# Performance work log

Measured on AMD Instinct MI355X. Metric: run time of the kernel, lower is better.

## Reference

```python
import jax, jax.numpy as jnp
import numpy as np

N, D_IN, D_OUT = 4096, 1024, 1024

def setup_inputs() -> dict:
    key = jax.random.key(0)
    ks = jax.random.split(key, 7)
    s = 1.0 / np.sqrt(D_IN)
    return {
        "x": jax.random.normal(ks[0], (N, D_IN), dtype=jnp.float32),
        "W1": jax.random.normal(ks[1], (D_OUT, D_IN), dtype=jnp.float32) * s,
        "b1": jax.random.normal(ks[2], (D_OUT,), dtype=jnp.float32) * 0.01,
        "W2": jax.random.normal(ks[3], (D_OUT, D_IN), dtype=jnp.float32) * s,
        "b2": jax.random.normal(ks[4], (D_OUT,), dtype=jnp.float32) * 0.01,
        "W3": jax.random.normal(ks[5], (D_OUT, D_IN), dtype=jnp.float32) * s,
        "b3": jax.random.normal(ks[6], (D_OUT,), dtype=jnp.float32) * 0.01,
        "output_dim": D_OUT,
    }

def reference(x, W1, b1, W2, b2, W3, b3, output_dim):
    # q, k, v: [N, D_OUT]  (torch Linear: x @ W.T + b)
    q = x @ W1.T + b1
    k = x @ W2.T + b2
    v = x @ W3.T + b3
    # NOTE: original computes K @ Q^T (not Q @ K^T) — keep faithful.
    scale = 1.0 / jnp.sqrt(jnp.asarray(output_dim, dtype=x.dtype))
    attn = jax.nn.softmax(jnp.einsum("nd,md->nm", k, q) * scale, axis=-1)  # [N, N]
    # value.unsqueeze(0) * attn.unsqueeze(-1) summed over axis 1 == attn @ v
    return attn @ v  # [N, D_OUT]
```

## Files before the change

kernel.cpp:

```cpp
#include <hip/hip_runtime.h>


typedef short bf16x8 __attribute__((ext_vector_type(8)));
typedef float f32x4  __attribute__((ext_vector_type(4)));

struct FalseT { static constexpr bool value = false; };
struct TrueT  { static constexpr bool value = true;  };

__device__ __forceinline__ short f2bf(float f) {
    unsigned u = __builtin_bit_cast(unsigned, f);
    u += 0x7FFFu + ((u >> 16) & 1u);
    return (short)(u >> 16);
}
__device__ __forceinline__ float bf2f(short s) {
    return __builtin_bit_cast(float, (unsigned)((unsigned short)s) << 16);
}

__device__ __forceinline__ void gld_lds16(const short* g, short* l) {
    __builtin_amdgcn_global_load_lds(
        (const __attribute__((address_space(1))) void*)g,
        (__attribute__((address_space(3))) void*)l, 16, 0, 0);
}

#define WAITV(n) asm volatile("s_waitcnt vmcnt(" #n ")" ::: "memory")
#define BAR()    __builtin_amdgcn_s_barrier()

template<int CMODE>
__global__ __launch_bounds__(512)
void gemm256(const short* __restrict__ A, int lda,
             const short* __restrict__ B, int ldb,
             const float* __restrict__ bias,
             short* __restrict__ Cout, int ldc, float scale,
             int K, size_t zstride)
{
    __shared__ __align__(16) short As[2][2][128 * 64];
    __shared__ __align__(16) short Bs[2][2][128 * 64];

    const int tid  = threadIdx.x;
    const int lane = tid & 63;
    const int wave = tid >> 6;
    const int wr   = wave >> 2;
    const int wc   = wave & 3;
    const int quad = lane >> 4;
    const int l16  = lane & 15;
    const size_t bm0 = (size_t)blockIdx.y * 256;
    const size_t bn0 = (size_t)blockIdx.x * 256;
    const int koff = blockIdx.z * K;

    f32x4 acc[8][4] = {};

    const int srow  = lane >> 3;
    const int sgran = (lane & 7) ^ srow;
    const short* Ag0 = A + (bm0 + wave * 16 + srow) * (size_t)lda + koff + sgran * 8;
    const short* Ag1 = Ag0 + (size_t)128 * lda;
    const short* Bg0 = B + (bn0 + wave * 16 + srow) * (size_t)ldb + koff + sgran * 8;
    const short* Bg1 = Bg0 + (size_t)128 * ldb;

    const int s0   = ((quad ^ (l16 & 7)) << 3);
    const int s1   = (((4 + quad) ^ (l16 & 7)) << 3);
    const int rdA0 = (wr * 64 + l16) * 64;
    const int rdB0 = (wc * 32 + l16) * 64;

    auto stage = [&](short* half, const short* g, int ld, int kt) {
#pragma unroll
        for (int i = 0; i < 2; ++i)
            gld_lds16(g + (size_t)(i * 8) * ld + kt,
                      half + (wave * 16 + i * 8) * 64);
    };

    bf16x8 af[4][2], bfr0[2][2], bfr1[2][2];

    auto ldA = [&](const short* Ah, int ks, int soff) {
#pragma unroll
        for (int m4 = 0; m4 < 4; ++m4)
            af[m4][ks] = *(const bf16x8*)(Ah + rdA0 + m4 * 1024 + soff);
    };
    auto ldB = [&](bf16x8 (&bx)[2][2], const short* Bh, int ks, int soff) {
#pragma unroll
        for (int n2 = 0; n2 < 2; ++n2)
            bx[n2][ks] = *(const bf16x8*)(Bh + rdB0 + n2 * 1024 + soff);
    };
    auto mmks = [&](int mq, int nq, bf16x8 (&bx)[2][2], int ks) {
#pragma unroll
        for (int m4 = 0; m4 < 4; ++m4)
#pragma unroll
            for (int n2 = 0; n2 < 2; ++n2)
                acc[mq * 4 + m4][nq * 2 + n2] =
                    __builtin_amdgcn_mfma_f32_16x16x32_bf16(
                        af[m4][ks], bx[n2][ks],
                        acc[mq * 4 + m4][nq * 2 + n2], 0, 0, 0);
    };

    stage(&As[0][0][0], Ag0, lda, 0);
    stage(&Bs[0][0][0], Bg0, ldb, 0);
    stage(&Bs[0][1][0], Bg1, ldb, 0);
    stage(&As[0][1][0], Ag1, lda, 0);
    stage(&As[1][0][0], Ag0, lda, 64);
    stage(&Bs[1][0][0], Bg0, ldb, 64);
    stage(&Bs[1][1][0], Bg1, ldb, 64);
    WAITV(6);
    BAR();
    __builtin_amdgcn_sched_barrier(0);

    int kt = 0;
    auto iterbody = [&](auto LASTC) {
        constexpr bool LAST = decltype(LASTC)::value;
        ldB(bfr0, &Bs[0][0][0], 0, s0);
        ldA(&As[0][0][0], 0, s0);
        ldB(bfr0, &Bs[0][0][0], 1, s1);
        ldA(&As[0][0][0], 1, s1);
        stage(&As[1][1][0], Ag1, lda, kt + 64);
        __builtin_amdgcn_s_setprio(1);
        mmks(0, 0, bfr0, 0); mmks(0, 0, bfr0, 1);
        __builtin_amdgcn_s_setprio(0);
        BAR();
        ldB(bfr1, &Bs[0][1][0], 0, s0);
        ldB(bfr1, &Bs[0][1][0], 1, s1);
        if constexpr (!LAST) stage(&As[0][0][0], Ag0, lda, kt + 128);
        __builtin_amdgcn_s_setprio(1);
        mmks(0, 1, bfr1, 0); mmks(0, 1, bfr1, 1);
        __builtin_amdgcn_s_setprio(0);
        BAR();
        ldA(&As[0][1][0], 0, s0);
        ldA(&As[0][1][0], 1, s1);
        if constexpr (!LAST) stage(&Bs[0][0][0], Bg0, ldb, kt + 128);
        __builtin_amdgcn_s_setprio(1);
        mmks(1, 1, bfr1, 0); mmks(1, 1, bfr1, 1);
        __builtin_amdgcn_s_setprio(0);
        BAR();
        if constexpr (!LAST) stage(&Bs[0][1][0], Bg1, ldb, kt + 128);
        __builtin_amdgcn_s_setprio(1);
        mmks(1, 0, bfr0, 0); mmks(1, 0, bfr0, 1);
        __builtin_amdgcn_s_setprio(0);
        if constexpr (LAST) { WAITV(0); } else { WAITV(6); }
        __builtin_amdgcn_sched_barrier(0);
        BAR();
        ldB(bfr0, &Bs[1][0][0], 0, s0);
        ldA(&As[1][0][0], 0, s0);
        ldB(bfr0, &Bs[1][0][0], 1, s1);
        ldA(&As[1][0][0], 1, s1);
        if constexpr (!LAST) stage(&As[0][1][0], Ag1, lda, kt + 128);
        __builtin_amdgcn_s_setprio(1);
        mmks(0, 0, bfr0, 0); mmks(0, 0, bfr0, 1);
        __builtin_amdgcn_s_setprio(0);
        BAR();
        ldB(bfr1, &Bs[1][1][0], 0, s0);
        ldB(bfr1, &Bs[1][1][0], 1, s1);
        if constexpr (!LAST) stage(&As[1][0][0], Ag0, lda, kt + 192);
        __builtin_amdgcn_s_setprio(1);
        mmks(0, 1, bfr1, 0); mmks(0, 1, bfr1, 1);
        __builtin_amdgcn_s_setprio(0);
        BAR();
        ldA(&As[1][1][0], 0, s0);
        ldA(&As[1][1][0], 1, s1);
        if constexpr (!LAST) stage(&Bs[1][0][0], Bg0, ldb, kt + 192);
        __builtin_amdgcn_s_setprio(1);
        mmks(1, 1, bfr1, 0); mmks(1, 1, bfr1, 1);
        __builtin_amdgcn_s_setprio(0);
        BAR();
        if constexpr (!LAST) stage(&Bs[1][1][0], Bg1, ldb, kt + 192);
        __builtin_amdgcn_s_setprio(1);
        mmks(1, 0, bfr0, 0); mmks(1, 0, bfr0, 1);
        __builtin_amdgcn_s_setprio(0);
        if constexpr (!LAST) {
            WAITV(6);
            __builtin_amdgcn_sched_barrier(0);
        }
        BAR();
    };

    const int nfull = (K >> 7) - 1;
    for (int i = 0; i < nfull; ++i) {
        iterbody(FalseT{});
        kt += 128;
    }
    iterbody(TrueT{});

    short* Cs = Cout + ((CMODE == 3) ? (size_t)blockIdx.z * zstride : 0);
#pragma unroll
    for (int mt = 0; mt < 8; ++mt) {
        const int mq = mt >> 2, m4 = mt & 3;
#pragma unroll
        for (int nt = 0; nt < 4; ++nt) {
            const int nq = nt >> 1, n2 = nt & 1;
            const size_t col = bn0 + nq * 128 + wc * 32 + n2 * 16 + l16;
            const float bc = (CMODE == 0) ? bias[col] : 0.0f;
#pragma unroll
            for (int r = 0; r < 4; ++r) {
                const size_t row = bm0 + mq * 128 + wr * 64 + m4 * 16 + quad * 4 + r;
                float v = acc[mt][nt][r] * scale + bc;
                if (CMODE == 2) v = __expf(v);
                Cs[row * (size_t)ldc + col] = f2bf(v);
            }
        }
    }
}

__global__ __launch_bounds__(256)
void transpose_v(const short* __restrict__ qkv, short* __restrict__ vt)
{
    __shared__ short sh[64][72];
    const int n0 = blockIdx.x * 64, d0 = blockIdx.y * 64;
    const int t = threadIdx.x;
    const int r = t >> 2, c = (t & 3) << 4;

    const short* src = qkv + (size_t)(n0 + r) * 3072 + 2048 + d0 + c;
    *(int4*)(&sh[r][c])     = *(const int4*)(src);
    *(int4*)(&sh[r][c + 8]) = *(const int4*)(src + 8);
    __syncthreads();

    short tmp[16];
#pragma unroll
    for (int j = 0; j < 16; j++) tmp[j] = sh[c + j][r];
    short* dst = vt + (size_t)(d0 + r) * 4096 + n0 + c;
    *(int4*)(dst)     = *(const int4*)(tmp);
    *(int4*)(dst + 8) = *(const int4*)(tmp + 8);
}

__global__ __launch_bounds__(256)
void reduce4div(const short* __restrict__ E, const short* __restrict__ outp,
                float* __restrict__ out)
{
    const int row = blockIdx.x;
    const int t = threadIdx.x;
    const int wave = t >> 6, lane = t & 63;

    const short* e = E + (size_t)row * 4096 + (t << 4);
    short sh[16];
    *(int4*)(sh)     = *(const int4*)(e);
    *(int4*)(sh + 8) = *(const int4*)(e + 8);
    float s = 0.0f;
#pragma unroll
    for (int i = 0; i < 16; i++) s += bf2f(sh[i]);
#pragma unroll
    for (int off = 32; off; off >>= 1) s += __shfl_down(s, off);
    __shared__ float red[4];
    if (lane == 0) red[wave] = s;
    __syncthreads();
    const float inv = 1.0f / (red[0] + red[1] + red[2] + red[3]);

    const size_t base = (size_t)row * 1024 + (t << 2);
    float a[4] = {0.0f, 0.0f, 0.0f, 0.0f};
#pragma unroll
    for (int z = 0; z < 4; z++) {
        short4 p = *(const short4*)(outp + z * (size_t)4096 * 1024 + base);
        a[0] += bf2f(p.x); a[1] += bf2f(p.y);
        a[2] += bf2f(p.z); a[3] += bf2f(p.w);
    }
    float4 o;
    o.x = a[0] * inv; o.y = a[1] * inv; o.z = a[2] * inv; o.w = a[3] * inv;
    *(float4*)(out + base) = o;
}

__global__ __launch_bounds__(256)
void prep(const float* __restrict__ x, const float* __restrict__ W1,
          const float* __restrict__ W2, const float* __restrict__ W3,
          const float* __restrict__ b1, const float* __restrict__ b2,
          const float* __restrict__ b3,
          short* __restrict__ xb, short* __restrict__ Wb,
          float* __restrict__ bcat)
{
    const int i = blockIdx.x * 256 + threadIdx.x;
    const int NX = 1048576;
    const int NW = 262144;
    if (i < NX + 3 * NW) {
        const float* src; short* dst; int j;
        if (i < NX)               { src = x;  dst = xb; j = i; }
        else if (i < NX + NW)     { src = W1; dst = Wb; j = i - NX; }
        else if (i < NX + 2 * NW) { src = W2; dst = Wb + 1048576; j = i - NX - NW; }
        else                      { src = W3; dst = Wb + 2097152; j = i - NX - 2 * NW; }
        const float4 f = ((const float4*)src)[j];
        short4 o;
        o.x = f2bf(f.x); o.y = f2bf(f.y); o.z = f2bf(f.z); o.w = f2bf(f.w);
        *(short4*)(dst + (j << 2)) = o;
    } else {
        const int j = i - (NX + 3 * NW);
        if (j < 3072)
            bcat[j] = (j < 1024) ? b1[j] : (j < 2048 ? b2[j - 1024] : b3[j - 2048]);
    }
}

extern "C" void kernel_launch(void* const* d_in, const int* in_sizes, int n_in,
                              void* d_out, int out_size, void* d_ws, size_t ws_size,
                              hipStream_t stream)
{
    const float* x  = (const float*)d_in[0];
    const float* W1 = (const float*)d_in[1];
    const float* b1 = (const float*)d_in[2];
    const float* W2 = (const float*)d_in[3];
    const float* b2 = (const float*)d_in[4];
    const float* W3 = (const float*)d_in[5];
    const float* b3 = (const float*)d_in[6];
    float* out = (float*)d_out;

    const int N = 4096, D = 1024;

    char* wsb = (char*)d_ws;
    short* vt   = (short*)wsb;
    short* E    = (short*)(wsb + (size_t)8  * 1024 * 1024);
    short* xb   = (short*)(wsb + (size_t)40 * 1024 * 1024);
    short* Wb   = (short*)(wsb + (size_t)48 * 1024 * 1024);
    float* bcat = (float*)(wsb + (size_t)54 * 1024 * 1024);
    short* qkv  = (short*)(wsb + (size_t)54 * 1024 * 1024 + 16384);
    short* outp = (short*)(wsb + (size_t)40 * 1024 * 1024);

    prep<<<(1048576 + 3 * 262144 + 3072 + 255) / 256, 256, 0, stream>>>(
        x, W1, W2, W3, b1, b2, b3, xb, Wb, bcat);

    dim3 gqkv(3 * D / 256, N / 256);
    gemm256<0><<<gqkv, 512, 0, stream>>>(xb, D, Wb, D, bcat,
                                         qkv, 3 * D, 1.0f, D, 0);

    dim3 gt(N / 64, D / 64);
    transpose_v<<<gt, 256, 0, stream>>>(qkv, vt);

    dim3 gs(N / 256, N / 256);
    gemm256<2><<<gs, 512, 0, stream>>>(qkv + D, 3 * D, qkv, 3 * D,
                                       nullptr, E, N, 0.03125f, D, 0);

    dim3 go(D / 256, N / 256, 4);
    gemm256<3><<<go, 512, 0, stream>>>(E, N, vt, N, nullptr,
                                       outp, D, 1.0f, N / 4,
                                       (size_t)N * D);

    reduce4div<<<N, 256, 0, stream>>>(E, outp, out);
}
```

Measured before the change: 212.9 us.

## Fuse softmax row sums into exp GEMM epilogue and double-buffer A fragments

The exp-score GEMM epilogue now accumulates per-row sums of the rounded bf16 exponentials, reduces them across the 16-lane group with shuffles, and atomically adds them into a row-sum buffer zeroed in the prep kernel. The final reduce kernel therefore no longer rereads the whole 4096x4096 E matrix to compute denominators. Separately, the main loop uses two A-fragment register sets so LDS reads for the next sub-tile can be issued before the current MFMAs. This adds float atomics (order-dependent sums) and more register pressure.

```diff
diff --git a/kernel.cpp b/kernel.cpp
--- a/kernel.cpp
+++ b/kernel.cpp
@@ -31,7 +31,7 @@
              const short* __restrict__ B, int ldb,
              const float* __restrict__ bias,
              short* __restrict__ Cout, int ldc, float scale,
-             int K, size_t zstride)
+             int K, size_t zstride, float* __restrict__ rsum)
 {
     __shared__ __align__(16) short As[2][2][128 * 64];
     __shared__ __align__(16) short Bs[2][2][128 * 64];
@@ -68,27 +68,31 @@
                       half + (wave * 16 + i * 8) * 64);
     };
 
-    bf16x8 af[4][2], bfr0[2][2], bfr1[2][2];
-
-    auto ldA = [&](const short* Ah, int ks, int soff) {
+    bf16x8 af0[4][2], af1[4][2], bfr0[2][2], bfr1[2][2];
+
+    auto ldA = [&](const short* Ah, int ks, int soff, bf16x8 (&dst)[4][2]) {
 #pragma unroll
         for (int m4 = 0; m4 < 4; ++m4)
-            af[m4][ks] = *(const bf16x8*)(Ah + rdA0 + m4 * 1024 + soff);
+            dst[m4][ks] = *(const bf16x8*)(Ah + rdA0 + m4 * 1024 + soff);
     };
     auto ldB = [&](bf16x8 (&bx)[2][2], const short* Bh, int ks, int soff) {
 #pragma unroll
         for (int n2 = 0; n2 < 2; ++n2)
             bx[n2][ks] = *(const bf16x8*)(Bh + rdB0 + n2 * 1024 + soff);
     };
-    auto mmks = [&](int mq, int nq, bf16x8 (&bx)[2][2], int ks) {
-#pragma unroll
-        for (int m4 = 0; m4 < 4; ++m4)
-#pragma unroll
-            for (int n2 = 0; n2 < 2; ++n2)
-                acc[mq * 4 + m4][nq * 2 + n2] =
-                    __builtin_amdgcn_mfma_f32_16x16x32_bf16(
-                        af[m4][ks], bx[n2][ks],
-                        acc[mq * 4 + m4][nq * 2 + n2], 0, 0, 0);
+    auto mm = [&](int mq, int nq, bf16x8 (&ax)[4][2], bf16x8 (&bx)[2][2]) {
+        __builtin_amdgcn_s_setprio(1);
+#pragma unroll
+        for (int ks = 0; ks < 2; ++ks)
+#pragma unroll
+            for (int m4 = 0; m4 < 4; ++m4)
+#pragma unroll
+                for (int n2 = 0; n2 < 2; ++n2)
+                    acc[mq * 4 + m4][nq * 2 + n2] =
+                        __builtin_amdgcn_mfma_f32_16x16x32_bf16(
+                            ax[m4][ks], bx[n2][ks],
+                            acc[mq * 4 + m4][nq * 2 + n2], 0, 0, 0);
+        __builtin_amdgcn_s_setprio(0);
     };
 
     stage(&As[0][0][0], Ag0, lda, 0);
@@ -106,62 +110,46 @@
     auto iterbody = [&](auto LASTC) {
         constexpr bool LAST = decltype(LASTC)::value;
         ldB(bfr0, &Bs[0][0][0], 0, s0);
-        ldA(&As[0][0][0], 0, s0);
+        ldA(&As[0][0][0], 0, s0, af0);
         ldB(bfr0, &Bs[0][0][0], 1, s1);
-        ldA(&As[0][0][0], 1, s1);
-        stage(&As[1][1][0], Ag1, lda, kt + 64);
-        __builtin_amdgcn_s_setprio(1);
-        mmks(0, 0, bfr0, 0); mmks(0, 0, bfr0, 1);
-        __builtin_amdgcn_s_setprio(0);
-        BAR();
+        ldA(&As[0][0][0], 1, s1, af0);
         ldB(bfr1, &Bs[0][1][0], 0, s0);
         ldB(bfr1, &Bs[0][1][0], 1, s1);
+        stage(&As[1][1][0], Ag1, lda, kt + 64);
+        mm(0, 0, af0, bfr0);
+        BAR();
+        ldA(&As[0][1][0], 0, s0, af1);
         if constexpr (!LAST) stage(&As[0][0][0], Ag0, lda, kt + 128);
-        __builtin_amdgcn_s_setprio(1);
-        mmks(0, 1, bfr1, 0); mmks(0, 1, bfr1, 1);
-        __builtin_amdgcn_s_setprio(0);
-        BAR();
-        ldA(&As[0][1][0], 0, s0);
-        ldA(&As[0][1][0], 1, s1);
+        mm(0, 1, af0, bfr1);
+        BAR();
+        ldA(&As[0][1][0], 1, s1, af1);
         if constexpr (!LAST) stage(&Bs[0][0][0], Bg0, ldb, kt + 128);
-        __builtin_amdgcn_s_setprio(1);
-        mmks(1, 1, bfr1, 0); mmks(1, 1, bfr1, 1);
-        __builtin_amdgcn_s_setprio(0);
+        mm(1, 1, af1, bfr1);
         BAR();
         if constexpr (!LAST) stage(&Bs[0][1][0], Bg1, ldb, kt + 128);
-        __builtin_amdgcn_s_setprio(1);
-        mmks(1, 0, bfr0, 0); mmks(1, 0, bfr0, 1);
-        __builtin_amdgcn_s_setprio(0);
+        mm(1, 0, af1, bfr0);
         if constexpr (LAST) { WAITV(0); } else { WAITV(6); }
         __builtin_amdgcn_sched_barrier(0);
         BAR();
         ldB(bfr0, &Bs[1][0][0], 0, s0);
-        ldA(&As[1][0][0], 0, s0);
+        ldA(&As[1][0][0], 0, s0, af0);
         ldB(bfr0, &Bs[1][0][0], 1, s1);
-        ldA(&As[1][0][0], 1, s1);
-        if constexpr (!LAST) stage(&As[0][1][0], Ag1, lda, kt + 128);
-        __builtin_amdgcn_s_setprio(1);
-        mmks(0, 0, bfr0, 0); mmks(0, 0, bfr0, 1);
-        __builtin_amdgcn_s_setprio(0);
-        BAR();
+        ldA(&As[1][0][0], 1, s1, af0);
         ldB(bfr1, &Bs[1][1][0], 0, s0);
         ldB(bfr1, &Bs[1][1][0], 1, s1);
+        if constexpr (!LAST) stage(&As[0][1][0], Ag1, lda, kt + 128);
+        mm(0, 0, af0, bfr0);
+        BAR();
+        ldA(&As[1][1][0], 0, s0, af1);
         if constexpr (!LAST) stage(&As[1][0][0], Ag0, lda, kt + 192);
-        __builtin_amdgcn_s_setprio(1);
-        mmks(0, 1, bfr1, 0); mmks(0, 1, bfr1, 1);
-        __builtin_amdgcn_s_setprio(0);
-        BAR();
-        ldA(&As[1][1][0], 0, s0);
-        ldA(&As[1][1][0], 1, s1);
+        mm(0, 1, af0, bfr1);
+        BAR();
+        ldA(&As[1][1][0], 1, s1, af1);
         if constexpr (!LAST) stage(&Bs[1][0][0], Bg0, ldb, kt + 192);
-        __builtin_amdgcn_s_setprio(1);
-        mmks(1, 1, bfr1, 0); mmks(1, 1, bfr1, 1);
-        __builtin_amdgcn_s_setprio(0);
+        mm(1, 1, af1, bfr1);
         BAR();
         if constexpr (!LAST) stage(&Bs[1][1][0], Bg1, ldb, kt + 192);
-        __builtin_amdgcn_s_setprio(1);
-        mmks(1, 0, bfr0, 0); mmks(1, 0, bfr0, 1);
-        __builtin_amdgcn_s_setprio(0);
+        mm(1, 0, af1, bfr0);
         if constexpr (!LAST) {
             WAITV(6);
             __builtin_amdgcn_sched_barrier(0);
@@ -181,16 +169,26 @@
     for (int mt = 0; mt < 8; ++mt) {
         const int mq = mt >> 2, m4 = mt & 3;
 #pragma unroll
-        for (int nt = 0; nt < 4; ++nt) {
-            const int nq = nt >> 1, n2 = nt & 1;
-            const size_t col = bn0 + nq * 128 + wc * 32 + n2 * 16 + l16;
-            const float bc = (CMODE == 0) ? bias[col] : 0.0f;
-#pragma unroll
-            for (int r = 0; r < 4; ++r) {
-                const size_t row = bm0 + mq * 128 + wr * 64 + m4 * 16 + quad * 4 + r;
-                float v = acc[mt][nt][r] * scale + bc;
+        for (int r = 0; r < 4; ++r) {
+            const size_t row = bm0 + mq * 128 + wr * 64 + m4 * 16 + quad * 4 + r;
+            float s = 0.0f;
+#pragma unroll
+            for (int nt = 0; nt < 4; ++nt) {
+                const int nq = nt >> 1, n2 = nt & 1;
+                const size_t col = bn0 + nq * 128 + wc * 32 + n2 * 16 + l16;
+                float v = acc[mt][nt][r] * scale +
+                          ((CMODE == 0) ? bias[col] : 0.0f);
                 if (CMODE == 2) v = __expf(v);
-                Cs[row * (size_t)ldc + col] = f2bf(v);
+                const short h = f2bf(v);
+                Cs[row * (size_t)ldc + col] = h;
+                if (CMODE == 2) s += bf2f(h);
+            }
+            if (CMODE == 2) {
+                s += __shfl_xor(s, 1);
+                s += __shfl_xor(s, 2);
+                s += __shfl_xor(s, 4);
+                s += __shfl_xor(s, 8);
+                if (l16 == 0) atomicAdd(&rsum[row], s);
             }
         }
     }
@@ -218,26 +216,12 @@
 }
 
 __global__ __launch_bounds__(256)
-void reduce4div(const short* __restrict__ E, const short* __restrict__ outp,
+void reduce4div(const float* __restrict__ rsum, const short* __restrict__ outp,
                 float* __restrict__ out)
 {
     const int row = blockIdx.x;
     const int t = threadIdx.x;
-    const int wave = t >> 6, lane = t & 63;
-
-    const short* e = E + (size_t)row * 4096 + (t << 4);
-    short sh[16];
-    *(int4*)(sh)     = *(const int4*)(e);
-    *(int4*)(sh + 8) = *(const int4*)(e + 8);
-    float s = 0.0f;
-#pragma unroll
-    for (int i = 0; i < 16; i++) s += bf2f(sh[i]);
-#pragma unroll
-    for (int off = 32; off; off >>= 1) s += __shfl_down(s, off);
-    __shared__ float red[4];
-    if (lane == 0) red[wave] = s;
-    __syncthreads();
-    const float inv = 1.0f / (red[0] + red[1] + red[2] + red[3]);
+    const float inv = 1.0f / rsum[row];
 
     const size_t base = (size_t)row * 1024 + (t << 2);
     float a[4] = {0.0f, 0.0f, 0.0f, 0.0f};
@@ -258,7 +242,7 @@
           const float* __restrict__ b1, const float* __restrict__ b2,
           const float* __restrict__ b3,
           short* __restrict__ xb, short* __restrict__ Wb,
-          float* __restrict__ bcat)
+          float* __restrict__ bcat, float* __restrict__ rsum)
 {
     const int i = blockIdx.x * 256 + threadIdx.x;
     const int NX = 1048576;
@@ -277,6 +261,8 @@
         const int j = i - (NX + 3 * NW);
         if (j < 3072)
             bcat[j] = (j < 1024) ? b1[j] : (j < 2048 ? b2[j - 1024] : b3[j - 2048]);
+        else if (j < 3072 + 4096)
+            rsum[j - 3072] = 0.0f;
     }
 }
 
@@ -303,25 +289,26 @@
     float* bcat = (float*)(wsb + (size_t)54 * 1024 * 1024);
     short* qkv  = (short*)(wsb + (size_t)54 * 1024 * 1024 + 16384);
     short* outp = (short*)(wsb + (size_t)40 * 1024 * 1024);
-
-    prep<<<(1048576 + 3 * 262144 + 3072 + 255) / 256, 256, 0, stream>>>(
-        x, W1, W2, W3, b1, b2, b3, xb, Wb, bcat);
+    float* rsum = (float*)(wsb + (size_t)79 * 1024 * 1024);
+
+    prep<<<(1048576 + 3 * 262144 + 3072 + 4096 + 255) / 256, 256, 0, stream>>>(
+        x, W1, W2, W3, b1, b2, b3, xb, Wb, bcat, rsum);
 
     dim3 gqkv(3 * D / 256, N / 256);
     gemm256<0><<<gqkv, 512, 0, stream>>>(xb, D, Wb, D, bcat,
-                                         qkv, 3 * D, 1.0f, D, 0);
+                                         qkv, 3 * D, 1.0f, D, 0, nullptr);
 
     dim3 gt(N / 64, D / 64);
     transpose_v<<<gt, 256, 0, stream>>>(qkv, vt);
 
     dim3 gs(N / 256, N / 256);
     gemm256<2><<<gs, 512, 0, stream>>>(qkv + D, 3 * D, qkv, 3 * D,
-                                       nullptr, E, N, 0.03125f, D, 0);
+                                       nullptr, E, N, 0.03125f, D, 0, rsum);
 
     dim3 go(D / 256, N / 256, 4);
     gemm256<3><<<go, 512, 0, stream>>>(E, N, vt, N, nullptr,
                                        outp, D, 1.0f, N / 4,
-                                       (size_t)N * D);
-
-    reduce4div<<<N, 256, 0, stream>>>(E, outp, out);
-}
+                                       (size_t)N * D, nullptr);
+
+    reduce4div<<<N, 256, 0, stream>>>(rsum, outp, out);
+}
```

Result: slower. 217.9 us (+2.3%).

## Fuse all six stages into one persistent cooperative kernel with grid syncs

Applied to the files above, without the earlier changes.

Replaces the six separate launches (convert, QKV GEMM, V transpose, score GEMM, PV GEMM, reduce/normalize) with one cooperative kernel of 256 blocks that runs each stage in turn and separates them with grid.sync. Work in each stage is remapped onto the fixed block count, and the QKV GEMM leaves 64 blocks idle. The aim is to remove per-launch overhead and the idle gaps between kernels. The cost is grid-wide barriers, lower parallelism in the light stages, and a kernel whose shared-memory and register footprint is sized for the GEMM.

```diff
diff --git a/kernel.cpp b/kernel.cpp
--- a/kernel.cpp
+++ b/kernel.cpp
@@ -1,4 +1,7 @@
 #include <hip/hip_runtime.h>
+#include <hip/hip_cooperative_groups.h>
+
+namespace cg = cooperative_groups;
 
 
 typedef short bf16x8 __attribute__((ext_vector_type(8)));
@@ -26,16 +29,14 @@
 #define BAR()    __builtin_amdgcn_s_barrier()
 
 template<int CMODE>
-__global__ __launch_bounds__(512)
-void gemm256(const short* __restrict__ A, int lda,
-             const short* __restrict__ B, int ldb,
-             const float* __restrict__ bias,
-             short* __restrict__ Cout, int ldc, float scale,
-             int K, size_t zstride)
+__device__ void gemm_body(short (&As)[2][2][128 * 64],
+                          short (&Bs)[2][2][128 * 64],
+                          const short* __restrict__ A, int lda,
+                          const short* __restrict__ B, int ldb,
+                          const float* __restrict__ bias,
+                          short* __restrict__ Cout, int ldc, float scale,
+                          int K, int bx, int by, int koff)
 {
-    __shared__ __align__(16) short As[2][2][128 * 64];
-    __shared__ __align__(16) short Bs[2][2][128 * 64];
-
     const int tid  = threadIdx.x;
     const int lane = tid & 63;
     const int wave = tid >> 6;
@@ -43,9 +44,8 @@
     const int wc   = wave & 3;
     const int quad = lane >> 4;
     const int l16  = lane & 15;
-    const size_t bm0 = (size_t)blockIdx.y * 256;
-    const size_t bn0 = (size_t)blockIdx.x * 256;
-    const int koff = blockIdx.z * K;
+    const size_t bm0 = (size_t)by * 256;
+    const size_t bn0 = (size_t)bx * 256;
 
     f32x4 acc[8][4] = {};
 
@@ -75,19 +75,19 @@
         for (int m4 = 0; m4 < 4; ++m4)
             af[m4][ks] = *(const bf16x8*)(Ah + rdA0 + m4 * 1024 + soff);
     };
-    auto ldB = [&](bf16x8 (&bx)[2][2], const short* Bh, int ks, int soff) {
+    auto ldB = [&](bf16x8 (&bx_)[2][2], const short* Bh, int ks, int soff) {
 #pragma unroll
         for (int n2 = 0; n2 < 2; ++n2)
-            bx[n2][ks] = *(const bf16x8*)(Bh + rdB0 + n2 * 1024 + soff);
-    };
-    auto mmks = [&](int mq, int nq, bf16x8 (&bx)[2][2], int ks) {
+            bx_[n2][ks] = *(const bf16x8*)(Bh + rdB0 + n2 * 1024 + soff);
+    };
+    auto mmks = [&](int mq, int nq, bf16x8 (&bx_)[2][2], int ks) {
 #pragma unroll
         for (int m4 = 0; m4 < 4; ++m4)
 #pragma unroll
             for (int n2 = 0; n2 < 2; ++n2)
                 acc[mq * 4 + m4][nq * 2 + n2] =
                     __builtin_amdgcn_mfma_f32_16x16x32_bf16(
-                        af[m4][ks], bx[n2][ks],
+                        af[m4][ks], bx_[n2][ks],
                         acc[mq * 4 + m4][nq * 2 + n2], 0, 0, 0);
     };
 
@@ -176,7 +176,6 @@
     }
     iterbody(TrueT{});
 
-    short* Cs = Cout + ((CMODE == 3) ? (size_t)blockIdx.z * zstride : 0);
 #pragma unroll
     for (int mt = 0; mt < 8; ++mt) {
         const int mq = mt >> 2, m4 = mt & 3;
@@ -190,93 +189,126 @@
                 const size_t row = bm0 + mq * 128 + wr * 64 + m4 * 16 + quad * 4 + r;
                 float v = acc[mt][nt][r] * scale + bc;
                 if (CMODE == 2) v = __expf(v);
-                Cs[row * (size_t)ldc + col] = f2bf(v);
+                Cout[row * (size_t)ldc + col] = f2bf(v);
             }
         }
     }
 }
 
-__global__ __launch_bounds__(256)
-void transpose_v(const short* __restrict__ qkv, short* __restrict__ vt)
+__global__ __launch_bounds__(512)
+void fused(const float* __restrict__ x, const float* __restrict__ W1,
+           const float* __restrict__ b1, const float* __restrict__ W2,
+           const float* __restrict__ b2, const float* __restrict__ W3,
+           const float* __restrict__ b3, float* __restrict__ out,
+           char* __restrict__ wsb)
 {
-    __shared__ short sh[64][72];
-    const int n0 = blockIdx.x * 64, d0 = blockIdx.y * 64;
-    const int t = threadIdx.x;
-    const int r = t >> 2, c = (t & 3) << 4;
-
-    const short* src = qkv + (size_t)(n0 + r) * 3072 + 2048 + d0 + c;
-    *(int4*)(&sh[r][c])     = *(const int4*)(src);
-    *(int4*)(&sh[r][c + 8]) = *(const int4*)(src + 8);
-    __syncthreads();
-
-    short tmp[16];
-#pragma unroll
-    for (int j = 0; j < 16; j++) tmp[j] = sh[c + j][r];
-    short* dst = vt + (size_t)(d0 + r) * 4096 + n0 + c;
-    *(int4*)(dst)     = *(const int4*)(tmp);
-    *(int4*)(dst + 8) = *(const int4*)(tmp + 8);
-}
-
-__global__ __launch_bounds__(256)
-void reduce4div(const short* __restrict__ E, const short* __restrict__ outp,
-                float* __restrict__ out)
-{
-    const int row = blockIdx.x;
-    const int t = threadIdx.x;
-    const int wave = t >> 6, lane = t & 63;
-
-    const short* e = E + (size_t)row * 4096 + (t << 4);
-    short sh[16];
-    *(int4*)(sh)     = *(const int4*)(e);
-    *(int4*)(sh + 8) = *(const int4*)(e + 8);
-    float s = 0.0f;
-#pragma unroll
-    for (int i = 0; i < 16; i++) s += bf2f(sh[i]);
-#pragma unroll
-    for (int off = 32; off; off >>= 1) s += __shfl_down(s, off);
-    __shared__ float red[4];
-    if (lane == 0) red[wave] = s;
-    __syncthreads();
-    const float inv = 1.0f / (red[0] + red[1] + red[2] + red[3]);
-
-    const size_t base = (size_t)row * 1024 + (t << 2);
-    float a[4] = {0.0f, 0.0f, 0.0f, 0.0f};
-#pragma unroll
-    for (int z = 0; z < 4; z++) {
-        short4 p = *(const short4*)(outp + z * (size_t)4096 * 1024 + base);
-        a[0] += bf2f(p.x); a[1] += bf2f(p.y);
-        a[2] += bf2f(p.z); a[3] += bf2f(p.w);
-    }
-    float4 o;
-    o.x = a[0] * inv; o.y = a[1] * inv; o.z = a[2] * inv; o.w = a[3] * inv;
-    *(float4*)(out + base) = o;
-}
-
-__global__ __launch_bounds__(256)
-void prep(const float* __restrict__ x, const float* __restrict__ W1,
-          const float* __restrict__ W2, const float* __restrict__ W3,
-          const float* __restrict__ b1, const float* __restrict__ b2,
-          const float* __restrict__ b3,
-          short* __restrict__ xb, short* __restrict__ Wb,
-          float* __restrict__ bcat)
-{
-    const int i = blockIdx.x * 256 + threadIdx.x;
-    const int NX = 1048576;
-    const int NW = 262144;
-    if (i < NX + 3 * NW) {
+    __shared__ __align__(16) short As[2][2][128 * 64];
+    __shared__ __align__(16) short Bs[2][2][128 * 64];
+
+    short* vt   = (short*)wsb;
+    short* E    = (short*)(wsb + (size_t)8  * 1024 * 1024);
+    short* xb   = (short*)(wsb + (size_t)40 * 1024 * 1024);
+    short* Wb   = (short*)(wsb + (size_t)48 * 1024 * 1024);
+    float* bcat = (float*)(wsb + (size_t)54 * 1024 * 1024);
+    short* qkv  = (short*)(wsb + (size_t)54 * 1024 * 1024 + 16384);
+    short* outp = (short*)(wsb + (size_t)40 * 1024 * 1024);
+
+    const int bid = blockIdx.x;
+    const int tid = threadIdx.x;
+    cg::grid_group grid = cg::this_grid();
+
+#pragma unroll 1
+    for (int it = 0; it < 14; ++it) {
+        const int i = it * 131072 + bid * 512 + tid;
         const float* src; short* dst; int j;
-        if (i < NX)               { src = x;  dst = xb; j = i; }
-        else if (i < NX + NW)     { src = W1; dst = Wb; j = i - NX; }
-        else if (i < NX + 2 * NW) { src = W2; dst = Wb + 1048576; j = i - NX - NW; }
-        else                      { src = W3; dst = Wb + 2097152; j = i - NX - 2 * NW; }
+        if (i < 1048576)      { src = x;  dst = xb;            j = i; }
+        else if (i < 1310720) { src = W1; dst = Wb;            j = i - 1048576; }
+        else if (i < 1572864) { src = W2; dst = Wb + 1048576;  j = i - 1310720; }
+        else                  { src = W3; dst = Wb + 2097152;  j = i - 1572864; }
         const float4 f = ((const float4*)src)[j];
         short4 o;
         o.x = f2bf(f.x); o.y = f2bf(f.y); o.z = f2bf(f.z); o.w = f2bf(f.w);
         *(short4*)(dst + (j << 2)) = o;
-    } else {
-        const int j = i - (NX + 3 * NW);
-        if (j < 3072)
-            bcat[j] = (j < 1024) ? b1[j] : (j < 2048 ? b2[j - 1024] : b3[j - 2048]);
+    }
+    {
+        const int g = bid * 512 + tid;
+        if (g < 3072)
+            bcat[g] = (g < 1024) ? b1[g] : (g < 2048 ? b2[g - 1024] : b3[g - 2048]);
+    }
+    grid.sync();
+
+    if (bid < 192) {
+        gemm_body<0>(As, Bs, xb, 1024, Wb, 1024, bcat,
+                     qkv, 3072, 1.0f, 1024, bid % 12, bid / 12, 0);
+    }
+    grid.sync();
+
+    {
+        short (*sh)[64][72] = (short (*)[64][72])&As[0][0][0];
+        const int half = tid >> 8;
+        const int tt = tid & 255;
+        const int r = tt >> 2, c = (tt & 3) << 4;
+#pragma unroll 1
+        for (int i2 = 0; i2 < 2; ++i2) {
+            const int t = bid * 4 + i2 * 2 + half;
+            const int n0 = (t & 63) * 64, d0 = (t >> 6) * 64;
+            const short* src = qkv + (size_t)(n0 + r) * 3072 + 2048 + d0 + c;
+            *(int4*)(&sh[half][r][c])     = *(const int4*)(src);
+            *(int4*)(&sh[half][r][c + 8]) = *(const int4*)(src + 8);
+            __syncthreads();
+            short tmp[16];
+#pragma unroll
+            for (int j = 0; j < 16; j++) tmp[j] = sh[half][c + j][r];
+            short* dst = vt + (size_t)(d0 + r) * 4096 + n0 + c;
+            *(int4*)(dst)     = *(const int4*)(tmp);
+            *(int4*)(dst + 8) = *(const int4*)(tmp + 8);
+            __syncthreads();
+        }
+    }
+    grid.sync();
+
+    gemm_body<2>(As, Bs, qkv + 1024, 3072, qkv, 3072, nullptr,
+                 E, 4096, 0.03125f, 1024, bid & 15, bid >> 4, 0);
+    grid.sync();
+
+    {
+        const int bz = bid >> 6;
+        gemm_body<3>(As, Bs, E, 4096, vt, 4096, nullptr,
+                     outp + (size_t)bz * 4194304, 1024, 1.0f, 1024,
+                     bid & 3, (bid >> 2) & 15, bz * 1024);
+    }
+    grid.sync();
+
+    {
+        float* red = (float*)&As[0][0][0];
+#pragma unroll 1
+        for (int rr = 0; rr < 16; ++rr) {
+            const int row = bid + rr * 256;
+            const short* e = E + (size_t)row * 4096 + tid * 8;
+            short sh8[8];
+            *(int4*)sh8 = *(const int4*)(e);
+            float s = 0.0f;
+#pragma unroll
+            for (int j = 0; j < 8; j++) s += bf2f(sh8[j]);
+#pragma unroll
+            for (int off = 32; off; off >>= 1) s += __shfl_down(s, off);
+            if ((tid & 63) == 0) red[tid >> 6] = s;
+            __syncthreads();
+            const float inv = 1.0f / (red[0] + red[1] + red[2] + red[3] +
+                                      red[4] + red[5] + red[6] + red[7]);
+            const size_t base = (size_t)row * 1024 + tid * 2;
+            float a0 = 0.0f, a1 = 0.0f;
+#pragma unroll
+            for (int z = 0; z < 4; z++) {
+                const int p = *(const int*)(outp + (size_t)z * 4194304 + base);
+                a0 += bf2f((short)(p & 0xffff));
+                a1 += bf2f((short)(((unsigned)p) >> 16));
+            }
+            float2 o2;
+            o2.x = a0 * inv; o2.y = a1 * inv;
+            *(float2*)(out + base) = o2;
+            __syncthreads();
+        }
     }
 }
 
@@ -292,36 +324,11 @@
     const float* W3 = (const float*)d_in[5];
     const float* b3 = (const float*)d_in[6];
     float* out = (float*)d_out;
-
-    const int N = 4096, D = 1024;
-
     char* wsb = (char*)d_ws;
-    short* vt   = (short*)wsb;
-    short* E    = (short*)(wsb + (size_t)8  * 1024 * 1024);
-    short* xb   = (short*)(wsb + (size_t)40 * 1024 * 1024);
-    short* Wb   = (short*)(wsb + (size_t)48 * 1024 * 1024);
-    float* bcat = (float*)(wsb + (size_t)54 * 1024 * 1024);
-    short* qkv  = (short*)(wsb + (size_t)54 * 1024 * 1024 + 16384);
-    short* outp = (short*)(wsb + (size_t)40 * 1024 * 1024);
-
-    prep<<<(1048576 + 3 * 262144 + 3072 + 255) / 256, 256, 0, stream>>>(
-        x, W1, W2, W3, b1, b2, b3, xb, Wb, bcat);
-
-    dim3 gqkv(3 * D / 256, N / 256);
-    gemm256<0><<<gqkv, 512, 0, stream>>>(xb, D, Wb, D, bcat,
-                                         qkv, 3 * D, 1.0f, D, 0);
-
-    dim3 gt(N / 64, D / 64);
-    transpose_v<<<gt, 256, 0, stream>>>(qkv, vt);
-
-    dim3 gs(N / 256, N / 256);
-    gemm256<2><<<gs, 512, 0, stream>>>(qkv + D, 3 * D, qkv, 3 * D,
-                                       nullptr, E, N, 0.03125f, D, 0);
-
-    dim3 go(D / 256, N / 256, 4);
-    gemm256<3><<<go, 512, 0, stream>>>(E, N, vt, N, nullptr,
-                                       outp, D, 1.0f, N / 4,
-                                       (size_t)N * D);
-
-    reduce4div<<<N, 256, 0, stream>>>(E, outp, out);
-}
+
+    void* args[] = { (void*)&x, (void*)&W1, (void*)&b1, (void*)&W2,
+                     (void*)&b2, (void*)&W3, (void*)&b3, (void*)&out,
+                     (void*)&wsb };
+    hipLaunchCooperativeKernel((const void*)fused, dim3(256), dim3(512),
+                               args, 0, stream);
+}
```

New measurement: 403.4 us. 89.5% more time.
